# Performance work log

Measured on AMD Instinct MI355X. Metric: run time of the kernel, lower is better.

Reference implementation:

```python
import jax, jax.numpy as jnp
import numpy as np

B, T, D, H = 4, 2048, 1024, 16
DH = D // H


def setup_inputs() -> dict:
    key = jax.random.key(0)
    ks = jax.random.split(key, 5)
    x = jax.random.normal(ks[0], (B, T, D), dtype=jnp.float32)
    W_qkv = jax.random.normal(ks[1], (D, 3 * D), dtype=jnp.float32) * 0.02
    b_qkv = jax.random.normal(ks[2], (3 * D,), dtype=jnp.float32) * 0.02
    W_o = jax.random.normal(ks[3], (D, D), dtype=jnp.float32) * 0.02
    b_o = jax.random.normal(ks[4], (D,), dtype=jnp.float32) * 0.02
    return {"x": x, "W_qkv": W_qkv, "b_qkv": b_qkv, "W_o": W_o, "b_o": b_o}


def reference(x, W_qkv, b_qkv, W_o, b_o):
    b, t, d = x.shape
    qkv = x @ W_qkv + b_qkv                      # [b, t, 3*d]
    # 'b t (k h dh) -> k b h t dh'
    qkv = qkv.reshape(b, t, 3, H, DH).transpose(2, 0, 3, 1, 4)
    q, k, v = qkv[0], qkv[1], qkv[2]             # each [b, h, t, dh]
    scores = jnp.einsum('bhqd,bhkd->bhqk', q, k) / jnp.sqrt(jnp.float32(DH))
    causal_mask = jnp.triu(jnp.ones((t, t), dtype=bool), k=1)  # True above diag
    scores = jnp.where(causal_mask, -jnp.inf, scores)
    attn = jax.nn.softmax(scores, axis=-1)       # [b, h, t, t]
    o = jnp.einsum('bhqk,bhkd->bqhd', attn, v).reshape(b, t, d)
    return o @ W_o + b_o
```

## Files before the change

kernel.cpp:

```cpp
#include <hip/hip_runtime.h>

typedef __attribute__((ext_vector_type(8))) short bh8;
typedef __attribute__((ext_vector_type(4))) float f32x4;

#define GBL(p) (const __attribute__((address_space(1))) void*)(p)
#define LDSP(p) (__attribute__((address_space(3))) void*)(p)

__device__ __forceinline__ ushort f2bf(float f){
  union { float f; unsigned u; } v; v.f = f;
  unsigned u = v.u;
  return (ushort)((u + 0x7fffu + ((u >> 16) & 1u)) >> 16);
}

__global__ __launch_bounds__(256) void cast_x_kernel(const float4* __restrict__ in,
                                                     ushort* __restrict__ out){
  int i = blockIdx.x * 256 + threadIdx.x;
  float4 v = in[i];
  ushort4 o;
  o.x = f2bf(v.x); o.y = f2bf(v.y); o.z = f2bf(v.z); o.w = f2bf(v.w);
  *(ushort4*)&out[(size_t)i * 4] = o;
}

__global__ __launch_bounds__(256) void transpose_cast_kernel(const float* __restrict__ in,
                                                             ushort* __restrict__ out,
                                                             int R, int C){
  __shared__ float tile[32][33];
  int bx = blockIdx.x * 32;
  int by = blockIdx.y * 32;
  int tx = threadIdx.x, ty = threadIdx.y;
  #pragma unroll
  for (int i = 0; i < 32; i += 8)
    tile[ty + i][tx] = in[(size_t)(by + ty + i) * C + bx + tx];
  __syncthreads();
  #pragma unroll
  for (int i = 0; i < 32; i += 8)
    out[(size_t)(bx + ty + i) * R + by + tx] = f2bf(tile[tx][ty + i]);
}

__global__ __launch_bounds__(256) void gemm_qkv_kernel(
    const ushort* __restrict__ A,
    const ushort* __restrict__ Bt,
    const float* __restrict__ bias,
    ushort* __restrict__ Qd, ushort* __restrict__ Kd, ushort* __restrict__ Vt)
{
  constexpr int K = 1024, BK = 32;
  __shared__ ushort sA[128 * BK];
  __shared__ ushort sB[128 * BK];
  const int tid = threadIdx.x;
  const int lane = tid & 63, wave = tid >> 6;
  const int quad = lane >> 4, l16 = lane & 15;
  const int wm = (wave >> 1) * 64, wn = (wave & 1) * 64;
  const size_t aBase = (size_t)blockIdx.x * 128 * K;
  const size_t bBase = (size_t)blockIdx.y * 128 * K;
  f32x4 acc[4][4] = {};
  for (int k0 = 0; k0 < K; k0 += BK){
    #pragma unroll
    for (int c = 0; c < 2; c++){
      int s = c * 256 + tid;
      __builtin_amdgcn_global_load_lds(GBL(A + aBase + (size_t)(s >> 2) * K + k0 + ((s & 3) << 3)),
                                       LDSP(&sA[s << 3]), 16, 0, 0);
      __builtin_amdgcn_global_load_lds(GBL(Bt + bBase + (size_t)(s >> 2) * K + k0 + ((s & 3) << 3)),
                                       LDSP(&sB[s << 3]), 16, 0, 0);
    }
    __syncthreads();
    bh8 af[4], bf[4];
    #pragma unroll
    for (int i = 0; i < 4; i++) af[i] = *(const bh8*)&sA[(wm + i * 16 + l16) * BK + quad * 8];
    #pragma unroll
    for (int j = 0; j < 4; j++) bf[j] = *(const bh8*)&sB[(wn + j * 16 + l16) * BK + quad * 8];
    #pragma unroll
    for (int i = 0; i < 4; i++)
      #pragma unroll
      for (int j = 0; j < 4; j++)
        acc[i][j] = __builtin_amdgcn_mfma_f32_16x16x32_bf16(af[i], bf[j], acc[i][j], 0, 0, 0);
    __syncthreads();
  }
  const int whichBlk = (blockIdx.y * 128) >> 10;
  #pragma unroll
  for (int i = 0; i < 4; i++){
    int mg = blockIdx.x * 128 + wm + i * 16 + quad * 4;
    int bb = mg >> 11, t0 = mg & 2047;
    #pragma unroll
    for (int j = 0; j < 4; j++){
      int ng = blockIdx.y * 128 + wn + j * 16 + l16;
      float bv = bias[ng];
      int h = (ng >> 6) & 15;
      int dh = ng & 63;
      if (whichBlk == 2){
        ushort4 o;
        o.x = f2bf(acc[i][j][0] + bv);
        o.y = f2bf(acc[i][j][1] + bv);
        o.z = f2bf(acc[i][j][2] + bv);
        o.w = f2bf(acc[i][j][3] + bv);
        *(ushort4*)&Vt[((size_t)((bb * 16 + h) * 64 + dh)) * 2048 + t0] = o;
      } else {
        ushort* dst = (whichBlk == 0) ? Qd : Kd;
        float sc = (whichBlk == 0) ? 0.125f : 1.0f;
        #pragma unroll
        for (int r = 0; r < 4; r++)
          dst[((size_t)((bb * 16 + h) * 2048 + t0 + r) << 6) + dh] = f2bf((acc[i][j][r] + bv) * sc);
      }
    }
  }
}

__global__ __launch_bounds__(256, 4) void flash_attn_kernel(
    const ushort* __restrict__ Qd, const ushort* __restrict__ Kd,
    const ushort* __restrict__ Vt, ushort* __restrict__ Od)
{
  __shared__ ushort sK[2][4096];
  __shared__ ushort sV[2][4096];
  __shared__ ushort sP[4][1024];
  const int tid = threadIdx.x;
  const int lane = tid & 63, wave = tid >> 6;
  const int quad = lane >> 4, l16 = lane & 15;
  const int pairI = blockIdx.x, bh = blockIdx.y;
  const size_t base = (size_t)bh * (2048 * 64);
  const float M = 5.0f;

  const int p0 = tid, p1 = 256 + tid;
  const int r0 = p0 >> 3, c0 = (p0 & 7) ^ (r0 & 7);
  const int r1 = p1 >> 3, c1 = (p1 & 7) ^ (r1 & 7);
  const ushort* kp0 = Kd + base + r0 * 64 + c0 * 8;
  const ushort* kp1 = Kd + base + r1 * 64 + c1 * 8;
  const ushort* vp0 = Vt + base + (size_t)r0 * 2048 + c0 * 8;
  const ushort* vp1 = Vt + base + (size_t)r1 * 2048 + c1 * 8;

  const int b = bh >> 4, h = bh & 15;

  #pragma unroll 1
  for (int phase = 0; phase < 2; phase++){
    const int qt = (phase == 0) ? (31 - pairI) : pairI;
    const ushort* qrow = Qd + base + (size_t)(qt * 64 + wave * 16 + l16) * 64 + quad * 8;
    bh8 qf0 = *(const bh8*)qrow;
    bh8 qf1 = *(const bh8*)(qrow + 32);

    f32x4 Oacc[4] = {};
    float lpart[4] = {0.f, 0.f, 0.f, 0.f};

    __syncthreads();
    __builtin_amdgcn_global_load_lds(GBL(kp0), LDSP(&sK[0][p0 * 8]), 16, 0, 0);
    __builtin_amdgcn_global_load_lds(GBL(kp1), LDSP(&sK[0][p1 * 8]), 16, 0, 0);
    __builtin_amdgcn_global_load_lds(GBL(vp0), LDSP(&sV[0][p0 * 8]), 16, 0, 0);
    __builtin_amdgcn_global_load_lds(GBL(vp1), LDSP(&sV[0][p1 * 8]), 16, 0, 0);

    #pragma unroll 1
    for (int kt = 0; kt <= qt; kt++){
      const int buf = kt & 1;
      __syncthreads();
      if (kt < qt){
        const int nb = buf ^ 1;
        __builtin_amdgcn_global_load_lds(GBL(kp0 + (kt + 1) * 4096), LDSP(&sK[nb][p0 * 8]), 16, 0, 0);
        __builtin_amdgcn_global_load_lds(GBL(kp1 + (kt + 1) * 4096), LDSP(&sK[nb][p1 * 8]), 16, 0, 0);
        __builtin_amdgcn_global_load_lds(GBL(vp0 + (kt + 1) * 64),   LDSP(&sV[nb][p0 * 8]), 16, 0, 0);
        __builtin_amdgcn_global_load_lds(GBL(vp1 + (kt + 1) * 64),   LDSP(&sV[nb][p1 * 8]), 16, 0, 0);
      }
      f32x4 S[4] = {};
      #pragma unroll
      for (int ks = 0; ks < 2; ks++){
        bh8 aq = ks ? qf1 : qf0;
        #pragma unroll
        for (int j = 0; j < 4; j++){
          int row = j * 16 + l16;
          int u = row * 8 + ((ks * 4 + quad) ^ (row & 7));
          bh8 bk = *(const bh8*)&sK[buf][u * 8];
          S[j] = __builtin_amdgcn_mfma_f32_16x16x32_bf16(aq, bk, S[j], 0, 0, 0);
        }
      }
      if (kt == qt){
        #pragma unroll
        for (int j = 0; j < 4; j++)
          #pragma unroll
          for (int r = 0; r < 4; r++){
            int qg = qt * 64 + wave * 16 + quad * 4 + r;
            int tg = kt * 64 + j * 16 + l16;
            if (tg > qg) S[j][r] = -1e30f;
          }
      }
      #pragma unroll
      for (int j = 0; j < 4; j++){
        #pragma unroll
        for (int r = 0; r < 4; r++){
          float p = __expf(S[j][r] - M);
          lpart[r] += p;
          int row = quad * 4 + r;
          int cu = 2 * j + (l16 >> 3);
          int phys = row * 8 + (cu ^ (row & 7));
          sP[wave][phys * 8 + (l16 & 7)] = f2bf(p);
        }
      }
      #pragma unroll
      for (int ks = 0; ks < 2; ks++){
        int up = l16 * 8 + ((ks * 4 + quad) ^ (l16 & 7));
        bh8 ap = *(const bh8*)&sP[wave][up * 8];
        #pragma unroll
        for (int j = 0; j < 4; j++){
          int row = j * 16 + l16;
          int u = row * 8 + ((ks * 4 + quad) ^ (row & 7));
          bh8 bv = *(const bh8*)&sV[buf][u * 8];
          Oacc[j] = __builtin_amdgcn_mfma_f32_16x16x32_bf16(ap, bv, Oacc[j], 0, 0, 0);
        }
      }
    }
    float lr[4];
    #pragma unroll
    for (int r = 0; r < 4; r++){
      float s = lpart[r];
      s += __shfl_xor(s, 1, 64);
      s += __shfl_xor(s, 2, 64);
      s += __shfl_xor(s, 4, 64);
      s += __shfl_xor(s, 8, 64);
      lr[r] = 1.0f / s;
    }
    #pragma unroll
    for (int j = 0; j < 4; j++)
      #pragma unroll
      for (int r = 0; r < 4; r++){
        int qg = qt * 64 + wave * 16 + quad * 4 + r;
        int dh = j * 16 + l16;
        Od[(size_t)(b * 2048 + qg) * 1024 + h * 64 + dh] = f2bf(Oacc[j][r] * lr[r]);
      }
  }
}

__global__ __launch_bounds__(256) void gemm_out_kernel(
    const ushort* __restrict__ A,
    const ushort* __restrict__ Bt,
    const float* __restrict__ bias,
    float* __restrict__ out)
{
  constexpr int K = 1024, BK = 32;
  __shared__ ushort sA[128 * BK];
  __shared__ ushort sB[128 * BK];
  const int tid = threadIdx.x;
  const int lane = tid & 63, wave = tid >> 6;
  const int quad = lane >> 4, l16 = lane & 15;
  const int wm = (wave >> 1) * 64, wn = (wave & 1) * 64;
  const size_t aBase = (size_t)blockIdx.x * 128 * K;
  const size_t bBase = (size_t)blockIdx.y * 128 * K;
  f32x4 acc[4][4] = {};
  for (int k0 = 0; k0 < K; k0 += BK){
    #pragma unroll
    for (int c = 0; c < 2; c++){
      int s = c * 256 + tid;
      __builtin_amdgcn_global_load_lds(GBL(A + aBase + (size_t)(s >> 2) * K + k0 + ((s & 3) << 3)),
                                       LDSP(&sA[s << 3]), 16, 0, 0);
      __builtin_amdgcn_global_load_lds(GBL(Bt + bBase + (size_t)(s >> 2) * K + k0 + ((s & 3) << 3)),
                                       LDSP(&sB[s << 3]), 16, 0, 0);
    }
    __syncthreads();
    bh8 af[4], bf[4];
    #pragma unroll
    for (int i = 0; i < 4; i++) af[i] = *(const bh8*)&sA[(wm + i * 16 + l16) * BK + quad * 8];
    #pragma unroll
    for (int j = 0; j < 4; j++) bf[j] = *(const bh8*)&sB[(wn + j * 16 + l16) * BK + quad * 8];
    #pragma unroll
    for (int i = 0; i < 4; i++)
      #pragma unroll
      for (int j = 0; j < 4; j++)
        acc[i][j] = __builtin_amdgcn_mfma_f32_16x16x32_bf16(af[i], bf[j], acc[i][j], 0, 0, 0);
    __syncthreads();
  }
  #pragma unroll
  for (int i = 0; i < 4; i++){
    int mg = blockIdx.x * 128 + wm + i * 16 + quad * 4;
    #pragma unroll
    for (int j = 0; j < 4; j++){
      int ng = blockIdx.y * 128 + wn + j * 16 + l16;
      float bv = bias[ng];
      #pragma unroll
      for (int r = 0; r < 4; r++)
        out[(size_t)(mg + r) * 1024 + ng] = acc[i][j][r] + bv;
    }
  }
}

extern "C" void kernel_launch(void* const* d_in, const int* in_sizes, int n_in,
                              void* d_out, int out_size, void* d_ws, size_t ws_size,
                              hipStream_t stream) {
  const float* x    = (const float*)d_in[0];
  const float* Wqkv = (const float*)d_in[1];
  const float* bqkv = (const float*)d_in[2];
  const float* Wo   = (const float*)d_in[3];
  const float* bo   = (const float*)d_in[4];
  float* out = (float*)d_out;

  char* p = (char*)d_ws;
  ushort* xb  = (ushort*)p;
  ushort* WqT = (ushort*)(p + 16777216);
  ushort* WoT = (ushort*)(p + 16777216 + 6291456);
  ushort* Qd  = (ushort*)(p + 25165824);
  ushort* Kd  = (ushort*)(p + 25165824 + 16777216);
  ushort* Vt  = (ushort*)(p + 25165824 + 33554432);
  ushort* Od  = xb;

  cast_x_kernel<<<8192, 256, 0, stream>>>((const float4*)x, xb);
  transpose_cast_kernel<<<dim3(96, 32), dim3(32, 8), 0, stream>>>(Wqkv, WqT, 1024, 3072);
  transpose_cast_kernel<<<dim3(32, 32), dim3(32, 8), 0, stream>>>(Wo, WoT, 1024, 1024);
  gemm_qkv_kernel<<<dim3(64, 24), 256, 0, stream>>>(xb, WqT, bqkv, Qd, Kd, Vt);
  flash_attn_kernel<<<dim3(16, 64), 256, 0, stream>>>(Qd, Kd, Vt, Od);
  gemm_out_kernel<<<dim3(64, 8), 256, 0, stream>>>(Od, WoT, bo, out);
}
```

Measured before the change: 272.7 us.

## Widen QKV GEMM K-step, 128-row flash query tiles, smaller out-proj tiles

The QKV GEMM now stages 64-wide K slices per barrier pair instead of 32, halving the synchronisation count. Flash attention processes two 64-row query sub-tiles per block (128 rows), reusing each K/V tile loaded into LDS for both, with the grid halved and occupancy hint lowered to 2. The output projection switches to 64x64 tiles with one 16-row strip per wave and more blocks, to raise parallelism for that small GEMM. Risks include higher register pressure in attention and fewer attention blocks, giving coarser load balance.

```diff
diff --git a/kernel.cpp b/kernel.cpp
--- a/kernel.cpp
+++ b/kernel.cpp
@@ -43,9 +43,9 @@
     const float* __restrict__ bias,
     ushort* __restrict__ Qd, ushort* __restrict__ Kd, ushort* __restrict__ Vt)
 {
-  constexpr int K = 1024, BK = 32;
-  __shared__ ushort sA[128 * BK];
-  __shared__ ushort sB[128 * BK];
+  constexpr int K = 1024;
+  __shared__ ushort sA[8192];
+  __shared__ ushort sB[8192];
   const int tid = threadIdx.x;
   const int lane = tid & 63, wave = tid >> 6;
   const int quad = lane >> 4, l16 = lane & 15;
@@ -53,26 +53,30 @@
   const size_t aBase = (size_t)blockIdx.x * 128 * K;
   const size_t bBase = (size_t)blockIdx.y * 128 * K;
   f32x4 acc[4][4] = {};
-  for (int k0 = 0; k0 < K; k0 += BK){
-    #pragma unroll
-    for (int c = 0; c < 2; c++){
-      int s = c * 256 + tid;
-      __builtin_amdgcn_global_load_lds(GBL(A + aBase + (size_t)(s >> 2) * K + k0 + ((s & 3) << 3)),
-                                       LDSP(&sA[s << 3]), 16, 0, 0);
-      __builtin_amdgcn_global_load_lds(GBL(Bt + bBase + (size_t)(s >> 2) * K + k0 + ((s & 3) << 3)),
-                                       LDSP(&sB[s << 3]), 16, 0, 0);
-    }
-    __syncthreads();
-    bh8 af[4], bf[4];
-    #pragma unroll
-    for (int i = 0; i < 4; i++) af[i] = *(const bh8*)&sA[(wm + i * 16 + l16) * BK + quad * 8];
-    #pragma unroll
-    for (int j = 0; j < 4; j++) bf[j] = *(const bh8*)&sB[(wn + j * 16 + l16) * BK + quad * 8];
-    #pragma unroll
-    for (int i = 0; i < 4; i++)
-      #pragma unroll
-      for (int j = 0; j < 4; j++)
-        acc[i][j] = __builtin_amdgcn_mfma_f32_16x16x32_bf16(af[i], bf[j], acc[i][j], 0, 0, 0);
+  for (int k0 = 0; k0 < K; k0 += 64){
+    #pragma unroll
+    for (int c = 0; c < 4; c++){
+      int u = c * 256 + tid;
+      int ks = u >> 9, row = (u >> 2) & 127, q = u & 3;
+      __builtin_amdgcn_global_load_lds(GBL(A + aBase + (size_t)row * K + k0 + ks * 32 + q * 8),
+                                       LDSP(&sA[u * 8]), 16, 0, 0);
+      __builtin_amdgcn_global_load_lds(GBL(Bt + bBase + (size_t)row * K + k0 + ks * 32 + q * 8),
+                                       LDSP(&sB[u * 8]), 16, 0, 0);
+    }
+    __syncthreads();
+    #pragma unroll
+    for (int ks = 0; ks < 2; ks++){
+      bh8 af[4], bf[4];
+      #pragma unroll
+      for (int i = 0; i < 4; i++) af[i] = *(const bh8*)&sA[ks * 4096 + (wm + i * 16 + l16) * 32 + quad * 8];
+      #pragma unroll
+      for (int j = 0; j < 4; j++) bf[j] = *(const bh8*)&sB[ks * 4096 + (wn + j * 16 + l16) * 32 + quad * 8];
+      #pragma unroll
+      for (int i = 0; i < 4; i++)
+        #pragma unroll
+        for (int j = 0; j < 4; j++)
+          acc[i][j] = __builtin_amdgcn_mfma_f32_16x16x32_bf16(af[i], bf[j], acc[i][j], 0, 0, 0);
+    }
     __syncthreads();
   }
   const int whichBlk = (blockIdx.y * 128) >> 10;
@@ -104,13 +108,13 @@
   }
 }
 
-__global__ __launch_bounds__(256, 4) void flash_attn_kernel(
+__global__ __launch_bounds__(256, 2) void flash_attn_kernel(
     const ushort* __restrict__ Qd, const ushort* __restrict__ Kd,
     const ushort* __restrict__ Vt, ushort* __restrict__ Od)
 {
   __shared__ ushort sK[2][4096];
   __shared__ ushort sV[2][4096];
-  __shared__ ushort sP[4][1024];
+  __shared__ ushort sP[4][2][1024];
   const int tid = threadIdx.x;
   const int lane = tid & 63, wave = tid >> 6;
   const int quad = lane >> 4, l16 = lane & 15;
@@ -130,13 +134,17 @@
 
   #pragma unroll 1
   for (int phase = 0; phase < 2; phase++){
-    const int qt = (phase == 0) ? (31 - pairI) : pairI;
-    const ushort* qrow = Qd + base + (size_t)(qt * 64 + wave * 16 + l16) * 64 + quad * 8;
-    bh8 qf0 = *(const bh8*)qrow;
-    bh8 qf1 = *(const bh8*)(qrow + 32);
-
-    f32x4 Oacc[4] = {};
-    float lpart[4] = {0.f, 0.f, 0.f, 0.f};
+    const int qt = phase ? pairI : (15 - pairI);
+    const int ktmax = 2 * qt + 1;
+    bh8 qf[2][2];
+    #pragma unroll
+    for (int s = 0; s < 2; s++){
+      const ushort* qrow = Qd + base + (size_t)(qt * 128 + s * 64 + wave * 16 + l16) * 64 + quad * 8;
+      qf[s][0] = *(const bh8*)qrow;
+      qf[s][1] = *(const bh8*)(qrow + 32);
+    }
+    f32x4 Oacc[2][4] = {};
+    float lpart[2][4] = {{0.f,0.f,0.f,0.f},{0.f,0.f,0.f,0.f}};
 
     __syncthreads();
     __builtin_amdgcn_global_load_lds(GBL(kp0), LDSP(&sK[0][p0 * 8]), 16, 0, 0);
@@ -145,133 +153,141 @@
     __builtin_amdgcn_global_load_lds(GBL(vp1), LDSP(&sV[0][p1 * 8]), 16, 0, 0);
 
     #pragma unroll 1
-    for (int kt = 0; kt <= qt; kt++){
+    for (int kt = 0; kt <= ktmax; kt++){
       const int buf = kt & 1;
       __syncthreads();
-      if (kt < qt){
+      if (kt < ktmax){
         const int nb = buf ^ 1;
         __builtin_amdgcn_global_load_lds(GBL(kp0 + (kt + 1) * 4096), LDSP(&sK[nb][p0 * 8]), 16, 0, 0);
         __builtin_amdgcn_global_load_lds(GBL(kp1 + (kt + 1) * 4096), LDSP(&sK[nb][p1 * 8]), 16, 0, 0);
         __builtin_amdgcn_global_load_lds(GBL(vp0 + (kt + 1) * 64),   LDSP(&sV[nb][p0 * 8]), 16, 0, 0);
         __builtin_amdgcn_global_load_lds(GBL(vp1 + (kt + 1) * 64),   LDSP(&sV[nb][p1 * 8]), 16, 0, 0);
       }
-      f32x4 S[4] = {};
+      const bool act0 = (kt < ktmax);
+      f32x4 S[2][4] = {};
       #pragma unroll
       for (int ks = 0; ks < 2; ks++){
-        bh8 aq = ks ? qf1 : qf0;
         #pragma unroll
         for (int j = 0; j < 4; j++){
           int row = j * 16 + l16;
           int u = row * 8 + ((ks * 4 + quad) ^ (row & 7));
           bh8 bk = *(const bh8*)&sK[buf][u * 8];
-          S[j] = __builtin_amdgcn_mfma_f32_16x16x32_bf16(aq, bk, S[j], 0, 0, 0);
+          if (act0) S[0][j] = __builtin_amdgcn_mfma_f32_16x16x32_bf16(qf[0][ks], bk, S[0][j], 0, 0, 0);
+          S[1][j] = __builtin_amdgcn_mfma_f32_16x16x32_bf16(qf[1][ks], bk, S[1][j], 0, 0, 0);
         }
       }
-      if (kt == qt){
+      if (kt >= ktmax - 1){
+        const int sd = (kt == ktmax) ? 1 : 0;
         #pragma unroll
         for (int j = 0; j < 4; j++)
           #pragma unroll
           for (int r = 0; r < 4; r++){
-            int qg = qt * 64 + wave * 16 + quad * 4 + r;
-            int tg = kt * 64 + j * 16 + l16;
-            if (tg > qg) S[j][r] = -1e30f;
+            int relq = wave * 16 + quad * 4 + r;
+            int relt = j * 16 + l16;
+            if (relt > relq) S[sd][j][r] = -1e30f;
           }
       }
       #pragma unroll
-      for (int j = 0; j < 4; j++){
-        #pragma unroll
-        for (int r = 0; r < 4; r++){
-          float p = __expf(S[j][r] - M);
-          lpart[r] += p;
-          int row = quad * 4 + r;
-          int cu = 2 * j + (l16 >> 3);
-          int phys = row * 8 + (cu ^ (row & 7));
-          sP[wave][phys * 8 + (l16 & 7)] = f2bf(p);
+      for (int s = 0; s < 2; s++){
+        if (s == 0 && !act0) continue;
+        #pragma unroll
+        for (int j = 0; j < 4; j++){
+          #pragma unroll
+          for (int r = 0; r < 4; r++){
+            float pv = __expf(S[s][j][r] - M);
+            lpart[s][r] += pv;
+            int row = quad * 4 + r;
+            int cu = 2 * j + (l16 >> 3);
+            int phys = row * 8 + (cu ^ (row & 7));
+            sP[wave][s][phys * 8 + (l16 & 7)] = f2bf(pv);
+          }
         }
       }
       #pragma unroll
       for (int ks = 0; ks < 2; ks++){
         int up = l16 * 8 + ((ks * 4 + quad) ^ (l16 & 7));
-        bh8 ap = *(const bh8*)&sP[wave][up * 8];
+        bh8 ap0, ap1;
+        if (act0) ap0 = *(const bh8*)&sP[wave][0][up * 8];
+        ap1 = *(const bh8*)&sP[wave][1][up * 8];
         #pragma unroll
         for (int j = 0; j < 4; j++){
           int row = j * 16 + l16;
           int u = row * 8 + ((ks * 4 + quad) ^ (row & 7));
           bh8 bv = *(const bh8*)&sV[buf][u * 8];
-          Oacc[j] = __builtin_amdgcn_mfma_f32_16x16x32_bf16(ap, bv, Oacc[j], 0, 0, 0);
+          if (act0) Oacc[0][j] = __builtin_amdgcn_mfma_f32_16x16x32_bf16(ap0, bv, Oacc[0][j], 0, 0, 0);
+          Oacc[1][j] = __builtin_amdgcn_mfma_f32_16x16x32_bf16(ap1, bv, Oacc[1][j], 0, 0, 0);
         }
       }
     }
-    float lr[4];
-    #pragma unroll
-    for (int r = 0; r < 4; r++){
-      float s = lpart[r];
-      s += __shfl_xor(s, 1, 64);
-      s += __shfl_xor(s, 2, 64);
-      s += __shfl_xor(s, 4, 64);
-      s += __shfl_xor(s, 8, 64);
-      lr[r] = 1.0f / s;
-    }
-    #pragma unroll
-    for (int j = 0; j < 4; j++)
+    #pragma unroll
+    for (int s = 0; s < 2; s++){
+      float lr[4];
       #pragma unroll
       for (int r = 0; r < 4; r++){
-        int qg = qt * 64 + wave * 16 + quad * 4 + r;
-        int dh = j * 16 + l16;
-        Od[(size_t)(b * 2048 + qg) * 1024 + h * 64 + dh] = f2bf(Oacc[j][r] * lr[r]);
-      }
-  }
-}
-
-__global__ __launch_bounds__(256) void gemm_out_kernel(
+        float sm = lpart[s][r];
+        sm += __shfl_xor(sm, 1, 64);
+        sm += __shfl_xor(sm, 2, 64);
+        sm += __shfl_xor(sm, 4, 64);
+        sm += __shfl_xor(sm, 8, 64);
+        lr[r] = 1.0f / sm;
+      }
+      #pragma unroll
+      for (int j = 0; j < 4; j++)
+        #pragma unroll
+        for (int r = 0; r < 4; r++){
+          int qg = qt * 128 + s * 64 + wave * 16 + quad * 4 + r;
+          int dh = j * 16 + l16;
+          Od[(size_t)(b * 2048 + qg) * 1024 + h * 64 + dh] = f2bf(Oacc[s][j][r] * lr[r]);
+        }
+    }
+  }
+}
+
+__global__ __launch_bounds__(256, 8) void gemm_out_kernel(
     const ushort* __restrict__ A,
     const ushort* __restrict__ Bt,
     const float* __restrict__ bias,
     float* __restrict__ out)
 {
-  constexpr int K = 1024, BK = 32;
-  __shared__ ushort sA[128 * BK];
-  __shared__ ushort sB[128 * BK];
+  constexpr int K = 1024;
+  __shared__ ushort sA[4096];
+  __shared__ ushort sB[4096];
   const int tid = threadIdx.x;
   const int lane = tid & 63, wave = tid >> 6;
   const int quad = lane >> 4, l16 = lane & 15;
-  const int wm = (wave >> 1) * 64, wn = (wave & 1) * 64;
-  const size_t aBase = (size_t)blockIdx.x * 128 * K;
-  const size_t bBase = (size_t)blockIdx.y * 128 * K;
-  f32x4 acc[4][4] = {};
-  for (int k0 = 0; k0 < K; k0 += BK){
+  const int wm = wave * 16;
+  const size_t aBase = (size_t)blockIdx.x * 64 * K;
+  const size_t bBase = (size_t)blockIdx.y * 64 * K;
+  f32x4 acc[4] = {};
+  for (int k0 = 0; k0 < K; k0 += 64){
     #pragma unroll
     for (int c = 0; c < 2; c++){
-      int s = c * 256 + tid;
-      __builtin_amdgcn_global_load_lds(GBL(A + aBase + (size_t)(s >> 2) * K + k0 + ((s & 3) << 3)),
-                                       LDSP(&sA[s << 3]), 16, 0, 0);
-      __builtin_amdgcn_global_load_lds(GBL(Bt + bBase + (size_t)(s >> 2) * K + k0 + ((s & 3) << 3)),
-                                       LDSP(&sB[s << 3]), 16, 0, 0);
-    }
-    __syncthreads();
-    bh8 af[4], bf[4];
-    #pragma unroll
-    for (int i = 0; i < 4; i++) af[i] = *(const bh8*)&sA[(wm + i * 16 + l16) * BK + quad * 8];
-    #pragma unroll
-    for (int j = 0; j < 4; j++) bf[j] = *(const bh8*)&sB[(wn + j * 16 + l16) * BK + quad * 8];
-    #pragma unroll
-    for (int i = 0; i < 4; i++)
-      #pragma unroll
-      for (int j = 0; j < 4; j++)
-        acc[i][j] = __builtin_amdgcn_mfma_f32_16x16x32_bf16(af[i], bf[j], acc[i][j], 0, 0, 0);
+      int u = c * 256 + tid;
+      int ks = u >> 8, row = (u >> 2) & 63, q = u & 3;
+      __builtin_amdgcn_global_load_lds(GBL(A + aBase + (size_t)row * K + k0 + ks * 32 + q * 8),
+                                       LDSP(&sA[u * 8]), 16, 0, 0);
+      __builtin_amdgcn_global_load_lds(GBL(Bt + bBase + (size_t)row * K + k0 + ks * 32 + q * 8),
+                                       LDSP(&sB[u * 8]), 16, 0, 0);
+    }
+    __syncthreads();
+    #pragma unroll
+    for (int ks = 0; ks < 2; ks++){
+      bh8 af = *(const bh8*)&sA[ks * 2048 + (wm + l16) * 32 + quad * 8];
+      #pragma unroll
+      for (int j = 0; j < 4; j++){
+        bh8 bf = *(const bh8*)&sB[ks * 2048 + (j * 16 + l16) * 32 + quad * 8];
+        acc[j] = __builtin_amdgcn_mfma_f32_16x16x32_bf16(af, bf, acc[j], 0, 0, 0);
+      }
+    }
     __syncthreads();
   }
   #pragma unroll
-  for (int i = 0; i < 4; i++){
-    int mg = blockIdx.x * 128 + wm + i * 16 + quad * 4;
-    #pragma unroll
-    for (int j = 0; j < 4; j++){
-      int ng = blockIdx.y * 128 + wn + j * 16 + l16;
-      float bv = bias[ng];
-      #pragma unroll
-      for (int r = 0; r < 4; r++)
-        out[(size_t)(mg + r) * 1024 + ng] = acc[i][j][r] + bv;
-    }
+  for (int j = 0; j < 4; j++){
+    int ng = blockIdx.y * 64 + j * 16 + l16;
+    float bv = bias[ng];
+    #pragma unroll
+    for (int r = 0; r < 4; r++)
+      out[(size_t)(blockIdx.x * 64 + wm + quad * 4 + r) * 1024 + ng] = acc[j][r] + bv;
   }
 }
 
@@ -298,6 +314,6 @@
   transpose_cast_kernel<<<dim3(96, 32), dim3(32, 8), 0, stream>>>(Wqkv, WqT, 1024, 3072);
   transpose_cast_kernel<<<dim3(32, 32), dim3(32, 8), 0, stream>>>(Wo, WoT, 1024, 1024);
   gemm_qkv_kernel<<<dim3(64, 24), 256, 0, stream>>>(xb, WqT, bqkv, Qd, Kd, Vt);
-  flash_attn_kernel<<<dim3(16, 64), 256, 0, stream>>>(Qd, Kd, Vt, Od);
-  gemm_out_kernel<<<dim3(64, 8), 256, 0, stream>>>(Od, WoT, bo, out);
-}
+  flash_attn_kernel<<<dim3(8, 64), 256, 0, stream>>>(Qd, Kd, Vt, Od);
+  gemm_out_kernel<<<dim3(128, 16), 256, 0, stream>>>(Od, WoT, bo, out);
+}
```

New measurement: 281.2 us. +3.1%, slower.
